# Kernel optimization log

Hardware: AMD Instinct MI355X
Metric: run time of the kernel (lower is better)

Reference implementation:

```python
import jax, jax.numpy as jnp
import numpy as np

N = 100000          # number of nodes (queries == sources here)
DEG = 32            # uniform neighbor count
E = N * DEG         # total edges
C_IN = 8
HID = 32
C_OUT = 32


def setup_inputs() -> dict:
    key = jax.random.key(0)
    k1, k2, k3, k4, k5 = jax.random.split(key, 5)
    in_features = jax.random.normal(k1, (N, C_IN), dtype=jnp.float32)
    in_weights = jax.random.uniform(k2, (N,), dtype=jnp.float32)
    # MLP: Linear(2*C_IN -> HID), GELU, Linear(HID -> C_OUT)
    W1 = jax.random.normal(k3, (2 * C_IN, HID), dtype=jnp.float32) / np.sqrt(2 * C_IN)
    b1 = jnp.zeros((HID,), dtype=jnp.float32)
    W2 = jax.random.normal(k4, (HID, C_OUT), dtype=jnp.float32) / np.sqrt(HID)
    b2 = jnp.zeros((C_OUT,), dtype=jnp.float32)
    neighbor_index = jax.random.randint(k5, (E,), 0, N, dtype=jnp.int64)
    row_splits = (jnp.arange(N + 1, dtype=jnp.int64) * DEG)  # uniform CSR splits
    return {"in_features": in_features, "in_weights": in_weights,
            "W1": W1, "b1": b1, "W2": W2, "b2": b2,
            "neighbor_index": neighbor_index, "row_splits": row_splits}


def reference(in_features, in_weights, W1, b1, W2, b2, neighbor_index, row_splits):
    num_edges = neighbor_index.shape[0]
    num_out = row_splits.shape[0] - 1  # M output nodes
    # segment id of each edge (== repeat_interleave of node ids by row counts)
    seg = jnp.searchsorted(row_splits, jnp.arange(num_edges), side="right") - 1
    gathered = in_features[neighbor_index]          # [E, C_in] neighbor gather
    self_feats = in_features[seg]                   # [E, C_in] repeated self features
    agg = jnp.concatenate([gathered, self_feats], axis=1)  # [E, 2*C_in]
    h = jax.nn.gelu(agg @ W1 + b1)                  # [E, HID]
    h = h @ W2 + b2                                 # [E, C_out]
    h = in_weights[neighbor_index][:, None] * h     # quadrature weighting
    sums = jax.ops.segment_sum(h, seg, num_segments=num_out)  # segment_csr sum
    counts = (row_splits[1:] - row_splits[:-1]).astype(h.dtype)
    out = sums / jnp.maximum(counts, 1)[:, None]    # reduce='mean'
    return out
```

## Files before the change

kernel.cpp:

```cpp
#include <hip/hip_runtime.h>

#define DEG 32
#define HID 32
#define CIN 8

typedef float v2f __attribute__((ext_vector_type(2)));
typedef short bf16x8 __attribute__((ext_vector_type(8)));
typedef float f32x16 __attribute__((ext_vector_type(16)));

#define GELU_A ((float)(2.0 * 1.4426950408889634 * 0.7978845608028654))
#define GELU_B ((float)(2.0 * 1.4426950408889634 * 0.7978845608028654 * 0.044715))

__device__ __forceinline__ unsigned f2bf(float f) {
    unsigned b = __float_as_uint(f);
    return (b + 0x7fffu + ((b >> 16) & 1u)) >> 16;
}
__device__ __forceinline__ unsigned pack2(float lo, float hi) {
    return f2bf(lo) | (f2bf(hi) << 16);
}

__global__ __launch_bounds__(256) void precompute_xw(
    const float* __restrict__ x, const float* __restrict__ W1,
    const float* __restrict__ W2, unsigned* __restrict__ x16,
    unsigned* __restrict__ w1f, unsigned* __restrict__ w2f, int N) {
    int tid = blockIdx.x * 256 + threadIdx.x;
    if (blockIdx.x == 0) {
        int t = threadIdx.x;
        if (t < 64) {
            int kb = (t >> 5) * 8, col = t & 31;
            uint4 o;
            o.x = pack2(W1[(kb + 0) * HID + col], W1[(kb + 1) * HID + col]);
            o.y = pack2(W1[(kb + 2) * HID + col], W1[(kb + 3) * HID + col]);
            o.z = pack2(W1[(kb + 4) * HID + col], W1[(kb + 5) * HID + col]);
            o.w = pack2(W1[(kb + 6) * HID + col], W1[(kb + 7) * HID + col]);
            *(uint4*)(w1f + t * 4) = o;
        } else if (t < 192) {
            int u = t - 64;
            int f = u >> 6, l = u & 63;
            int kb = f * 16 + ((l >> 5) * 8), col = l & 31;
            uint4 o;
            o.x = pack2(W2[(kb + 0) * HID + col], W2[(kb + 1) * HID + col]);
            o.y = pack2(W2[(kb + 2) * HID + col], W2[(kb + 3) * HID + col]);
            o.z = pack2(W2[(kb + 4) * HID + col], W2[(kb + 5) * HID + col]);
            o.w = pack2(W2[(kb + 6) * HID + col], W2[(kb + 7) * HID + col]);
            *(uint4*)(w2f + (f * 64 + l) * 4) = o;
        }
    }
    if (tid < N) {
        const float4* xp = (const float4*)(x + (size_t)tid * CIN);
        float4 a = xp[0], b = xp[1];
        uint4 o;
        o.x = pack2(a.x, a.y);  o.y = pack2(a.z, a.w);
        o.z = pack2(b.x, b.y);  o.w = pack2(b.z, b.w);
        *(uint4*)(x16 + (size_t)tid * 4) = o;
    }
}

__device__ __forceinline__ float gelu_reduce(const f32x16& acc, const float* swp,
                                             float b1v) {
    float4 wq0 = *(const float4*)(swp);
    float4 wq1 = *(const float4*)(swp + 8);
    float4 wq2 = *(const float4*)(swp + 16);
    float4 wq3 = *(const float4*)(swp + 24);
    float wqa[16] = {wq0.x, wq0.y, wq0.z, wq0.w,  wq1.x, wq1.y, wq1.z, wq1.w,
                     wq2.x, wq2.y, wq2.z, wq2.w,  wq3.x, wq3.y, wq3.z, wq3.w};
    v2f gacc = {0.f, 0.f};
#pragma unroll
    for (int i = 0; i < 16; i += 2) {
        v2f tt = {acc[i] + b1v, acc[i + 1] + b1v};
        v2f x2 = tt * tt;
        v2f zz = tt * (x2 * (-GELU_B) + (-GELU_A));
        v2f ee;
        ee.x = __builtin_amdgcn_exp2f(zz.x);  ee.y = __builtin_amdgcn_exp2f(zz.y);
        v2f dd = ee + 1.0f;
        v2f rr;
        rr.x = __builtin_amdgcn_rcpf(dd.x);   rr.y = __builtin_amdgcn_rcpf(dd.y);
        v2f wp = {wqa[i], wqa[i + 1]};
        gacc += wp * (tt * rr);
    }
    float g = gacc.x + gacc.y;
    g += __shfl_xor(g, 32);
    return g;
}

__global__ __launch_bounds__(256, 5) void git_fused(
    const unsigned* __restrict__ x16, const unsigned* __restrict__ w1f,
    const unsigned* __restrict__ w2f, const float* __restrict__ wgt,
    const float* __restrict__ b1, const float* __restrict__ b2,
    const int* __restrict__ nbr, float* __restrict__ out, int N) {
    __shared__ float          sw[8 * DEG];
    __shared__ unsigned short sg[32 * 40];
    __shared__ float          sws[32];

    int t = threadIdx.x;
    int wv = t >> 6;
    int l  = t & 63;
    int l5 = l & 31;
    int hi = l >> 5;
    int nb = blockIdx.x * 8 + wv * 2;

    int jn[2]; float w[2]; int ncl[2];
#pragma unroll
    for (int r = 0; r < 2; ++r) {
        int n = nb + r; ncl[r] = n < N ? n : (N - 1);
        jn[r] = nbr[ncl[r] * DEG + l5];
        w[r]  = wgt[jn[r]];
    }
    if (hi == 0) {
#pragma unroll
        for (int r = 0; r < 2; ++r) sw[(wv * 2 + r) * DEG + l5] = w[r];
    }

    float ws[2];
#pragma unroll
    for (int r = 0; r < 2; ++r) {
        float s = w[r];
        s += __shfl_xor(s, 1);  s += __shfl_xor(s, 2);
        s += __shfl_xor(s, 4);  s += __shfl_xor(s, 8);
        s += __shfl_xor(s, 16);
        ws[r] = s;
    }

    bf16x8 af0 = *((const bf16x8*)x16 + (hi ? ncl[0] : jn[0]));
    bf16x8 af1 = *((const bf16x8*)x16 + (hi ? ncl[1] : jn[1]));
    bf16x8 bf  = *((const bf16x8*)w1f + l);
    float myb1 = b1[l5];

    f32x16 z0 = {}, z1 = {};
    f32x16 a0 = __builtin_amdgcn_mfma_f32_32x32x16_bf16(af0, bf, z0, 0, 0, 0);
    f32x16 a1 = __builtin_amdgcn_mfma_f32_32x32x16_bf16(af1, bf, z1, 0, 0, 0);

    const float* swb = &sw[wv * 2 * DEG + hi * 4];
    float g0 = gelu_reduce(a0, swb, myb1);
    float g1 = gelu_reduce(a1, swb + DEG, myb1);

    if (hi == 0) {
        sg[(wv * 2 + 0) * 40 + l5] = (unsigned short)f2bf(g0);
        sg[(wv * 2 + 1) * 40 + l5] = (unsigned short)f2bf(g1);
        if (l5 == 0) { sws[wv * 2] = ws[0]; sws[wv * 2 + 1] = ws[1]; }
    }

    __syncthreads();

    if (wv != 0) return;

    const char* sgb = (const char*)sg;
    bf16x8 ea1 = *(const bf16x8*)(sgb + l5 * 80 + hi * 16);
    bf16x8 ea2 = *(const bf16x8*)(sgb + l5 * 80 + 32 + hi * 16);
    bf16x8 eb1 = *((const bf16x8*)w2f + l);
    bf16x8 eb2 = *((const bf16x8*)w2f + 64 + l);

    f32x16 zz = {};
    f32x16 acc = __builtin_amdgcn_mfma_f32_32x32x16_bf16(ea1, eb1, zz, 0, 0, 0);
    acc = __builtin_amdgcn_mfma_f32_32x32x16_bf16(ea2, eb2, acc, 0, 0, 0);

    float myb2 = b2[l5];
    float4 wsq = *(const float4*)(sws + hi * 4);
    float wsa[4] = {wsq.x, wsq.y, wsq.z, wsq.w};

#pragma unroll
    for (int i = 0; i < 4; ++i) {
        int r = i + 4 * hi;
        int node = blockIdx.x * 8 + r;
        if (node < N)
            out[(size_t)node * HID + l5] = fmaf(wsa[i], myb2, acc[i]) * (1.0f / DEG);
    }
}

__global__ __launch_bounds__(256) void fused_fallback(
    const float* __restrict__ x, const float* __restrict__ wgt,
    const float* __restrict__ W1, const float* __restrict__ b1,
    const float* __restrict__ W2, const float* __restrict__ b2,
    const int* __restrict__ nbr, float* __restrict__ out, int N) {
    __shared__ float sW2[HID * HID];
    __shared__ float sb2[HID];
    __shared__ int2  sp[8 * DEG];
    int t = threadIdx.x;
#pragma unroll
    for (int i = 0; i < 4; ++i) sW2[t + i * 256] = W2[t + i * 256];
    if (t < HID) sb2[t] = b2[t];
    int slot = t >> 5, hid = t & 31;
    int node = blockIdx.x * 8 + slot;
    bool valid = node < N;
    int nc = valid ? node : (N - 1);
    int   j_own = nbr[nc * DEG + hid];
    float w_own = wgt[j_own];
    sp[slot * DEG + hid] = make_int2(j_own * (CIN * 4), __float_as_int(w_own));
    const float4* xip = (const float4*)(x + (size_t)nc * CIN);
    float4 xa = xip[0], xb = xip[1];
    float w1t[8];
#pragma unroll
    for (int k = 0; k < 8; ++k) w1t[k] = W1[k * HID + hid];
    float vb = b1[hid];
    vb = fmaf(xa.x, W1[ 8 * HID + hid], vb);
    vb = fmaf(xa.y, W1[ 9 * HID + hid], vb);
    vb = fmaf(xa.z, W1[10 * HID + hid], vb);
    vb = fmaf(xa.w, W1[11 * HID + hid], vb);
    vb = fmaf(xb.x, W1[12 * HID + hid], vb);
    vb = fmaf(xb.y, W1[13 * HID + hid], vb);
    vb = fmaf(xb.z, W1[14 * HID + hid], vb);
    vb = fmaf(xb.w, W1[15 * HID + hid], vb);
    float ws = w_own;
    ws += __shfl_xor(ws, 1);  ws += __shfl_xor(ws, 2);
    ws += __shfl_xor(ws, 4);  ws += __shfl_xor(ws, 8);
    ws += __shfl_xor(ws, 16);
    __syncthreads();
    const char* xbytes = (const char*)x;
    const int2* myp = &sp[slot * DEG];
    float g = 0.f;
#pragma unroll 8
    for (int e = 0; e < DEG; ++e) {
        int2  p  = myp[e];
        float wjv = __int_as_float(p.y);
        const float4* xjp = (const float4*)(xbytes + (unsigned)p.x);
        float4 a = xjp[0], b = xjp[1];
        float tin = vb;
        tin = fmaf(a.x, w1t[0], tin); tin = fmaf(a.y, w1t[1], tin);
        tin = fmaf(a.z, w1t[2], tin); tin = fmaf(a.w, w1t[3], tin);
        tin = fmaf(b.x, w1t[4], tin); tin = fmaf(b.y, w1t[5], tin);
        tin = fmaf(b.z, w1t[6], tin); tin = fmaf(b.w, w1t[7], tin);
        float x2 = tin * tin;
        float z  = tin * fmaf(GELU_B, x2, GELU_A);
        float e2 = __builtin_amdgcn_exp2f(z);
        float r  = __builtin_amdgcn_rcpf(1.0f + e2);
        g = fmaf(wjv, fmaf(-tin, r, tin), g);
    }
    float acc = 0.f;
#pragma unroll
    for (int h = 0; h < HID; ++h) {
        float gh = __shfl(g, h, 32);
        acc = fmaf(gh, sW2[h * HID + hid], acc);
    }
    if (valid) out[(size_t)node * HID + hid] = fmaf(ws, sb2[hid], acc) * (1.0f / DEG);
}

extern "C" void kernel_launch(void* const* d_in, const int* in_sizes, int n_in,
                              void* d_out, int out_size, void* d_ws, size_t ws_size,
                              hipStream_t stream) {
    const float* x   = (const float*)d_in[0];
    const float* wq  = (const float*)d_in[1];
    const float* W1  = (const float*)d_in[2];
    const float* b1  = (const float*)d_in[3];
    const float* W2  = (const float*)d_in[4];
    const float* b2  = (const float*)d_in[5];
    const int*   nbr = (const int*)d_in[6];
    float* out = (float*)d_out;

    int N = in_sizes[1];

    size_t off_x16 = 0;
    size_t off_w1  = (off_x16 + (size_t)N * 16 + 255) & ~(size_t)255;
    size_t off_w2  = off_w1 + 1024;
    size_t need    = off_w2 + 2048;

    if (ws_size >= need) {
        unsigned* x16 = (unsigned*)((char*)d_ws + off_x16);
        unsigned* w1f = (unsigned*)((char*)d_ws + off_w1);
        unsigned* w2f = (unsigned*)((char*)d_ws + off_w2);

        int blocks_pre = (N + 255) / 256;
        precompute_xw<<<blocks_pre, 256, 0, stream>>>(x, W1, W2, x16, w1f, w2f, N);

        int blocks_main = (N + 7) / 8;
        git_fused<<<blocks_main, 256, 0, stream>>>(x16, w1f, w2f, wq, b1, b2,
                                                   nbr, out, N);
    } else {
        int blocks = (N + 7) / 8;
        fused_fallback<<<blocks, 256, 0, stream>>>(x, wq, W1, b1, W2, b2, nbr, out, N);
    }
}
```

Measured before the change: 113.0 us.

## Make git_fused a persistent grid-stride kernel with prefetch and double-buffered LDS

The fused kernel now runs on a capped grid of 2048 blocks. Each block loops over 8-node groups in grid-stride order. While it computes the current group, it issues the neighbor-index, weight and feature gathers for the next group and the index load for the one after. The shared-memory buffers for the second MLP stage are double-buffered, and the wave that does the second-stage MFMA rotates per group, so one barrier per iteration is enough. The aim is to hide gather latency and avoid per-block launch and setup cost, in exchange for more live registers and dropping the min-waves occupancy hint.

Result: slower. 119.6 us (+5.8%).

```diff
diff --git a/kernel.cpp b/kernel.cpp
--- a/kernel.cpp
+++ b/kernel.cpp
@@ -58,112 +58,137 @@
 
 __device__ __forceinline__ float gelu_reduce(const f32x16& acc, const float* swp,
                                              float b1v) {
-    float4 wq0 = *(const float4*)(swp);
-    float4 wq1 = *(const float4*)(swp + 8);
-    float4 wq2 = *(const float4*)(swp + 16);
-    float4 wq3 = *(const float4*)(swp + 24);
-    float wqa[16] = {wq0.x, wq0.y, wq0.z, wq0.w,  wq1.x, wq1.y, wq1.z, wq1.w,
-                     wq2.x, wq2.y, wq2.z, wq2.w,  wq3.x, wq3.y, wq3.z, wq3.w};
     v2f gacc = {0.f, 0.f};
 #pragma unroll
-    for (int i = 0; i < 16; i += 2) {
-        v2f tt = {acc[i] + b1v, acc[i + 1] + b1v};
-        v2f x2 = tt * tt;
-        v2f zz = tt * (x2 * (-GELU_B) + (-GELU_A));
-        v2f ee;
-        ee.x = __builtin_amdgcn_exp2f(zz.x);  ee.y = __builtin_amdgcn_exp2f(zz.y);
-        v2f dd = ee + 1.0f;
-        v2f rr;
-        rr.x = __builtin_amdgcn_rcpf(dd.x);   rr.y = __builtin_amdgcn_rcpf(dd.y);
-        v2f wp = {wqa[i], wqa[i + 1]};
-        gacc += wp * (tt * rr);
+    for (int q = 0; q < 4; ++q) {
+        float4 wq = *(const float4*)(swp + 8 * q);
+#pragma unroll
+        for (int h = 0; h < 2; ++h) {
+            int i = q * 4 + h * 2;
+            v2f tt = {acc[i] + b1v, acc[i + 1] + b1v};
+            v2f x2 = tt * tt;
+            v2f zz = tt * (x2 * (-GELU_B) + (-GELU_A));
+            v2f ee;
+            ee.x = __builtin_amdgcn_exp2f(zz.x);  ee.y = __builtin_amdgcn_exp2f(zz.y);
+            v2f dd = ee + 1.0f;
+            v2f rr;
+            rr.x = __builtin_amdgcn_rcpf(dd.x);   rr.y = __builtin_amdgcn_rcpf(dd.y);
+            v2f wp = h ? (v2f){wq.z, wq.w} : (v2f){wq.x, wq.y};
+            gacc += wp * (tt * rr);
+        }
     }
     float g = gacc.x + gacc.y;
     g += __shfl_xor(g, 32);
     return g;
 }
 
-__global__ __launch_bounds__(256, 5) void git_fused(
+__global__ __launch_bounds__(256) void git_fused(
     const unsigned* __restrict__ x16, const unsigned* __restrict__ w1f,
     const unsigned* __restrict__ w2f, const float* __restrict__ wgt,
     const float* __restrict__ b1, const float* __restrict__ b2,
     const int* __restrict__ nbr, float* __restrict__ out, int N) {
-    __shared__ float          sw[8 * DEG];
-    __shared__ unsigned short sg[32 * 40];
-    __shared__ float          sws[32];
-
+    __shared__ float sw[8 * DEG];
+    __shared__ __align__(16) unsigned short sg[2][32 * 40];
+    __shared__ __align__(16) float          sws[2][8];
+
+    const int ngroups = (N + 7) >> 3;
     int t = threadIdx.x;
     int wv = t >> 6;
     int l  = t & 63;
     int l5 = l & 31;
     int hi = l >> 5;
-    int nb = blockIdx.x * 8 + wv * 2;
-
-    int jn[2]; float w[2]; int ncl[2];
-#pragma unroll
-    for (int r = 0; r < 2; ++r) {
-        int n = nb + r; ncl[r] = n < N ? n : (N - 1);
-        jn[r] = nbr[ncl[r] * DEG + l5];
-        w[r]  = wgt[jn[r]];
-    }
-    if (hi == 0) {
-#pragma unroll
-        for (int r = 0; r < 2; ++r) sw[(wv * 2 + r) * DEG + l5] = w[r];
-    }
-
-    float ws[2];
-#pragma unroll
-    for (int r = 0; r < 2; ++r) {
-        float s = w[r];
-        s += __shfl_xor(s, 1);  s += __shfl_xor(s, 2);
-        s += __shfl_xor(s, 4);  s += __shfl_xor(s, 8);
-        s += __shfl_xor(s, 16);
-        ws[r] = s;
-    }
-
-    bf16x8 af0 = *((const bf16x8*)x16 + (hi ? ncl[0] : jn[0]));
-    bf16x8 af1 = *((const bf16x8*)x16 + (hi ? ncl[1] : jn[1]));
-    bf16x8 bf  = *((const bf16x8*)w1f + l);
-    float myb1 = b1[l5];
-
-    f32x16 z0 = {}, z1 = {};
-    f32x16 a0 = __builtin_amdgcn_mfma_f32_32x32x16_bf16(af0, bf, z0, 0, 0, 0);
-    f32x16 a1 = __builtin_amdgcn_mfma_f32_32x32x16_bf16(af1, bf, z1, 0, 0, 0);
-
-    const float* swb = &sw[wv * 2 * DEG + hi * 4];
-    float g0 = gelu_reduce(a0, swb, myb1);
-    float g1 = gelu_reduce(a1, swb + DEG, myb1);
-
-    if (hi == 0) {
-        sg[(wv * 2 + 0) * 40 + l5] = (unsigned short)f2bf(g0);
-        sg[(wv * 2 + 1) * 40 + l5] = (unsigned short)f2bf(g1);
-        if (l5 == 0) { sws[wv * 2] = ws[0]; sws[wv * 2 + 1] = ws[1]; }
-    }
-
-    __syncthreads();
-
-    if (wv != 0) return;
-
-    const char* sgb = (const char*)sg;
-    bf16x8 ea1 = *(const bf16x8*)(sgb + l5 * 80 + hi * 16);
-    bf16x8 ea2 = *(const bf16x8*)(sgb + l5 * 80 + 32 + hi * 16);
-    bf16x8 eb1 = *((const bf16x8*)w2f + l);
-    bf16x8 eb2 = *((const bf16x8*)w2f + 64 + l);
-
-    f32x16 zz = {};
-    f32x16 acc = __builtin_amdgcn_mfma_f32_32x32x16_bf16(ea1, eb1, zz, 0, 0, 0);
-    acc = __builtin_amdgcn_mfma_f32_32x32x16_bf16(ea2, eb2, acc, 0, 0, 0);
-
-    float myb2 = b2[l5];
-    float4 wsq = *(const float4*)(sws + hi * 4);
-    float wsa[4] = {wsq.x, wsq.y, wsq.z, wsq.w};
-
-#pragma unroll
-    for (int i = 0; i < 4; ++i) {
-        int r = i + 4 * hi;
-        int node = blockIdx.x * 8 + r;
-        if (node < N)
-            out[(size_t)node * HID + l5] = fmaf(wsa[i], myb2, acc[i]) * (1.0f / DEG);
+
+    bf16x8 bfrag = *((const bf16x8*)w1f + l);
+    bf16x8 eb1   = *((const bf16x8*)w2f + l);
+    bf16x8 eb2   = *((const bf16x8*)w2f + 64 + l);
+    float  myb1  = b1[l5];
+    float  myb2  = b2[l5];
+    const bf16x8* x16v = (const bf16x8*)x16;
+
+    int g = blockIdx.x;
+    const int gstep = gridDim.x;
+    if (g >= ngroups) return;
+
+    int nb0 = g * 8 + wv * 2;
+    int n0c = min(nb0, N - 1), n1c = min(nb0 + 1, N - 1);
+    int   J = nbr[(hi ? n1c : n0c) * DEG + l5];
+    float W = wgt[J];
+    int jsw = __shfl_xor(J, 32);
+    bf16x8 A0 = x16v[hi ? n0c : J];
+    bf16x8 A1 = x16v[hi ? n1c : jsw];
+
+    int gn = g + gstep;
+    int Jn = 0;
+    if (gn < ngroups) {
+        int nbn = gn * 8 + wv * 2;
+        Jn = nbr[min(nbn + hi, N - 1) * DEG + l5];
+    }
+
+    int p = 0;
+    while (true) {
+        bf16x8 A0n, A1n;
+        float  Wn = 0.f;
+        int gn2 = gn + gstep;
+        int Jn2 = 0;
+        if (gn < ngroups) {
+            int nbn = gn * 8 + wv * 2;
+            int n0n = min(nbn, N - 1), n1n = min(nbn + 1, N - 1);
+            Wn = wgt[Jn];
+            int jswn = __shfl_xor(Jn, 32);
+            A0n = x16v[hi ? n0n : Jn];
+            A1n = x16v[hi ? n1n : jswn];
+            if (gn2 < ngroups) {
+                Jn2 = nbr[min(gn2 * 8 + wv * 2 + hi, N - 1) * DEG + l5];
+            }
+        }
+
+        float ws = W;
+        ws += __shfl_xor(ws, 1);  ws += __shfl_xor(ws, 2);
+        ws += __shfl_xor(ws, 4);  ws += __shfl_xor(ws, 8);
+        ws += __shfl_xor(ws, 16);
+        sw[(wv * 2 + hi) * DEG + l5] = W;
+        if (l5 == 0) sws[p][wv * 2 + hi] = ws;
+
+        f32x16 z0 = {}, z1 = {};
+        f32x16 a0 = __builtin_amdgcn_mfma_f32_32x32x16_bf16(A0, bfrag, z0, 0, 0, 0);
+        f32x16 a1 = __builtin_amdgcn_mfma_f32_32x32x16_bf16(A1, bfrag, z1, 0, 0, 0);
+
+        const float* swb = &sw[wv * 2 * DEG + hi * 4];
+        float g0 = gelu_reduce(a0, swb, myb1);
+        float g1 = gelu_reduce(a1, swb + DEG, myb1);
+
+        if (hi == 0) {
+            sg[p][(wv * 2 + 0) * 40 + l5] = (unsigned short)f2bf(g0);
+            sg[p][(wv * 2 + 1) * 40 + l5] = (unsigned short)f2bf(g1);
+        }
+
+        __syncthreads();
+
+        if (wv == (g & 3)) {
+            const char* sgb = (const char*)sg[p];
+            bf16x8 ea1 = *(const bf16x8*)(sgb + l5 * 80 + hi * 16);
+            bf16x8 ea2 = *(const bf16x8*)(sgb + l5 * 80 + 32 + hi * 16);
+            f32x16 zz = {};
+            f32x16 acc = __builtin_amdgcn_mfma_f32_32x32x16_bf16(ea1, eb1, zz, 0, 0, 0);
+            acc = __builtin_amdgcn_mfma_f32_32x32x16_bf16(ea2, eb2, acc, 0, 0, 0);
+
+            float4 wsq = *(const float4*)(&sws[p][hi * 4]);
+            float wsa[4] = {wsq.x, wsq.y, wsq.z, wsq.w};
+#pragma unroll
+            for (int i = 0; i < 4; ++i) {
+                int r = i + 4 * hi;
+                int node = g * 8 + r;
+                if (node < N)
+                    out[(size_t)node * HID + l5] =
+                        fmaf(wsa[i], myb2, acc[i]) * (1.0f / DEG);
+            }
+        }
+
+        if (gn >= ngroups) break;
+        g = gn;  gn = gn2;
+        J = Jn;  Jn = Jn2;
+        W = Wn;  A0 = A0n;  A1 = A1n;
+        p ^= 1;
     }
 }
 
@@ -261,7 +286,8 @@
         int blocks_pre = (N + 255) / 256;
         precompute_xw<<<blocks_pre, 256, 0, stream>>>(x, W1, W2, x16, w1f, w2f, N);
 
-        int blocks_main = (N + 7) / 8;
+        int ngroups = (N + 7) / 8;
+        int blocks_main = ngroups < 2048 ? ngroups : 2048;
         git_fused<<<blocks_main, 256, 0, stream>>>(x16, w1f, w2f, wq, b1, b2,
                                                    nbr, out, N);
     } else {
```

## Give each wave four nodes and do the second MLP layer per wave without block sync

Applied to the files above, without the earlier changes.

Each wavefront now handles four output nodes instead of two, using both 32-lane halves to load neighbor indices for different nodes, so the block covers 16 nodes. The second-layer MFMA is done per wave from wave-private shared memory, which removes the __syncthreads and the idle waves that previously exited while wave 0 finished alone. W2 fragments and biases are hoisted to the start, and launch bounds drop to 4 blocks per SM. In exchange each wave does more MFMA and output work and holds more registers, and occupancy may fall.

Measured after the change: 115.8 us. 1.02x slower.

```diff
diff --git a/kernel.cpp b/kernel.cpp
--- a/kernel.cpp
+++ b/kernel.cpp
@@ -58,112 +58,116 @@
 
 __device__ __forceinline__ float gelu_reduce(const f32x16& acc, const float* swp,
                                              float b1v) {
-    float4 wq0 = *(const float4*)(swp);
-    float4 wq1 = *(const float4*)(swp + 8);
-    float4 wq2 = *(const float4*)(swp + 16);
-    float4 wq3 = *(const float4*)(swp + 24);
-    float wqa[16] = {wq0.x, wq0.y, wq0.z, wq0.w,  wq1.x, wq1.y, wq1.z, wq1.w,
-                     wq2.x, wq2.y, wq2.z, wq2.w,  wq3.x, wq3.y, wq3.z, wq3.w};
     v2f gacc = {0.f, 0.f};
 #pragma unroll
-    for (int i = 0; i < 16; i += 2) {
-        v2f tt = {acc[i] + b1v, acc[i + 1] + b1v};
-        v2f x2 = tt * tt;
-        v2f zz = tt * (x2 * (-GELU_B) + (-GELU_A));
-        v2f ee;
-        ee.x = __builtin_amdgcn_exp2f(zz.x);  ee.y = __builtin_amdgcn_exp2f(zz.y);
-        v2f dd = ee + 1.0f;
-        v2f rr;
-        rr.x = __builtin_amdgcn_rcpf(dd.x);   rr.y = __builtin_amdgcn_rcpf(dd.y);
-        v2f wp = {wqa[i], wqa[i + 1]};
-        gacc += wp * (tt * rr);
+    for (int q = 0; q < 4; ++q) {
+        float4 wq = *(const float4*)(swp + 8 * q);
+#pragma unroll
+        for (int h = 0; h < 2; ++h) {
+            int i = q * 4 + h * 2;
+            v2f tt = {acc[i] + b1v, acc[i + 1] + b1v};
+            v2f x2 = tt * tt;
+            v2f zz = tt * (x2 * (-GELU_B) + (-GELU_A));
+            v2f ee;
+            ee.x = __builtin_amdgcn_exp2f(zz.x);  ee.y = __builtin_amdgcn_exp2f(zz.y);
+            v2f dd = ee + 1.0f;
+            v2f rr;
+            rr.x = __builtin_amdgcn_rcpf(dd.x);   rr.y = __builtin_amdgcn_rcpf(dd.y);
+            v2f wp = h ? (v2f){wq.z, wq.w} : (v2f){wq.x, wq.y};
+            gacc += wp * (tt * rr);
+        }
     }
     float g = gacc.x + gacc.y;
     g += __shfl_xor(g, 32);
     return g;
 }
 
-__global__ __launch_bounds__(256, 5) void git_fused(
+__global__ __launch_bounds__(256, 4) void git_fused(
     const unsigned* __restrict__ x16, const unsigned* __restrict__ w1f,
     const unsigned* __restrict__ w2f, const float* __restrict__ wgt,
     const float* __restrict__ b1, const float* __restrict__ b2,
     const int* __restrict__ nbr, float* __restrict__ out, int N) {
-    __shared__ float          sw[8 * DEG];
-    __shared__ unsigned short sg[32 * 40];
-    __shared__ float          sws[32];
+    __shared__ float sw[4 * 4 * 32];
+    __shared__ __align__(16) unsigned short sg[1792];
 
     int t = threadIdx.x;
     int wv = t >> 6;
     int l  = t & 63;
     int l5 = l & 31;
     int hi = l >> 5;
-    int nb = blockIdx.x * 8 + wv * 2;
-
-    int jn[2]; float w[2]; int ncl[2];
-#pragma unroll
-    for (int r = 0; r < 2; ++r) {
-        int n = nb + r; ncl[r] = n < N ? n : (N - 1);
-        jn[r] = nbr[ncl[r] * DEG + l5];
-        w[r]  = wgt[jn[r]];
-    }
-    if (hi == 0) {
-#pragma unroll
-        for (int r = 0; r < 2; ++r) sw[(wv * 2 + r) * DEG + l5] = w[r];
-    }
-
-    float ws[2];
-#pragma unroll
-    for (int r = 0; r < 2; ++r) {
-        float s = w[r];
-        s += __shfl_xor(s, 1);  s += __shfl_xor(s, 2);
-        s += __shfl_xor(s, 4);  s += __shfl_xor(s, 8);
-        s += __shfl_xor(s, 16);
-        ws[r] = s;
-    }
-
-    bf16x8 af0 = *((const bf16x8*)x16 + (hi ? ncl[0] : jn[0]));
-    bf16x8 af1 = *((const bf16x8*)x16 + (hi ? ncl[1] : jn[1]));
-    bf16x8 bf  = *((const bf16x8*)w1f + l);
+    int nb = blockIdx.x * 16 + wv * 4;
+
+    int n0 = min(nb + 0, N - 1), n1 = min(nb + 1, N - 1);
+    int n2 = min(nb + 2, N - 1), n3 = min(nb + 3, N - 1);
+
+    int JA = nbr[(hi ? n1 : n0) * DEG + l5];
+    int JB = nbr[(hi ? n3 : n2) * DEG + l5];
+    float WA = wgt[JA];
+    float WB = wgt[JB];
+    int jswA = __shfl_xor(JA, 32);
+    int jswB = __shfl_xor(JB, 32);
+
+    const bf16x8* x16v = (const bf16x8*)x16;
+    bf16x8 A0 = x16v[hi ? n0 : JA];
+    bf16x8 A1 = x16v[hi ? n1 : jswA];
+    bf16x8 A2 = x16v[hi ? n2 : JB];
+    bf16x8 A3 = x16v[hi ? n3 : jswB];
+    bf16x8 bfrag = *((const bf16x8*)w1f + l);
+    bf16x8 eb1   = *((const bf16x8*)w2f + l);
+    bf16x8 eb2   = *((const bf16x8*)w2f + 64 + l);
     float myb1 = b1[l5];
+    float myb2 = b2[l5];
+
+    float* swv = &sw[wv * 128];
+    swv[hi * 32 + l5]      = WA;
+    swv[64 + hi * 32 + l5] = WB;
+
+    float wsA = WA, wsB = WB;
+    wsA += __shfl_xor(wsA, 1);  wsA += __shfl_xor(wsA, 2);
+    wsA += __shfl_xor(wsA, 4);  wsA += __shfl_xor(wsA, 8);
+    wsA += __shfl_xor(wsA, 16);
+    wsB += __shfl_xor(wsB, 1);  wsB += __shfl_xor(wsB, 2);
+    wsB += __shfl_xor(wsB, 4);  wsB += __shfl_xor(wsB, 8);
+    wsB += __shfl_xor(wsB, 16);
 
     f32x16 z0 = {}, z1 = {};
-    f32x16 a0 = __builtin_amdgcn_mfma_f32_32x32x16_bf16(af0, bf, z0, 0, 0, 0);
-    f32x16 a1 = __builtin_amdgcn_mfma_f32_32x32x16_bf16(af1, bf, z1, 0, 0, 0);
-
-    const float* swb = &sw[wv * 2 * DEG + hi * 4];
-    float g0 = gelu_reduce(a0, swb, myb1);
-    float g1 = gelu_reduce(a1, swb + DEG, myb1);
-
-    if (hi == 0) {
-        sg[(wv * 2 + 0) * 40 + l5] = (unsigned short)f2bf(g0);
-        sg[(wv * 2 + 1) * 40 + l5] = (unsigned short)f2bf(g1);
-        if (l5 == 0) { sws[wv * 2] = ws[0]; sws[wv * 2 + 1] = ws[1]; }
-    }
-
-    __syncthreads();
-
-    if (wv != 0) return;
-
-    const char* sgb = (const char*)sg;
+    f32x16 a0 = __builtin_amdgcn_mfma_f32_32x32x16_bf16(A0, bfrag, z0, 0, 0, 0);
+    f32x16 a1 = __builtin_amdgcn_mfma_f32_32x32x16_bf16(A1, bfrag, z1, 0, 0, 0);
+    float g0 = gelu_reduce(a0, swv + hi * 4,      myb1);
+    float g1 = gelu_reduce(a1, swv + 32 + hi * 4, myb1);
+    f32x16 z2 = {}, z3 = {};
+    f32x16 a2 = __builtin_amdgcn_mfma_f32_32x32x16_bf16(A2, bfrag, z2, 0, 0, 0);
+    f32x16 a3 = __builtin_amdgcn_mfma_f32_32x32x16_bf16(A3, bfrag, z3, 0, 0, 0);
+    float g2 = gelu_reduce(a2, swv + 64 + hi * 4, myb1);
+    float g3 = gelu_reduce(a3, swv + 96 + hi * 4, myb1);
+
+    unsigned short* sgw = &sg[wv * 160];
+    float ga = hi ? g2 : g0;
+    float gb = hi ? g3 : g1;
+    sgw[(2 * hi + 0) * 40 + l5] = (unsigned short)f2bf(ga);
+    sgw[(2 * hi + 1) * 40 + l5] = (unsigned short)f2bf(gb);
+
+    float wsa[4];
+    wsa[0] = __shfl(wsA, 0);
+    wsa[1] = __shfl(wsA, 32);
+    wsa[2] = __shfl(wsB, 0);
+    wsa[3] = __shfl(wsB, 32);
+
+    const char* sgb = (const char*)sgw;
     bf16x8 ea1 = *(const bf16x8*)(sgb + l5 * 80 + hi * 16);
     bf16x8 ea2 = *(const bf16x8*)(sgb + l5 * 80 + 32 + hi * 16);
-    bf16x8 eb1 = *((const bf16x8*)w2f + l);
-    bf16x8 eb2 = *((const bf16x8*)w2f + 64 + l);
-
     f32x16 zz = {};
     f32x16 acc = __builtin_amdgcn_mfma_f32_32x32x16_bf16(ea1, eb1, zz, 0, 0, 0);
     acc = __builtin_amdgcn_mfma_f32_32x32x16_bf16(ea2, eb2, acc, 0, 0, 0);
 
-    float myb2 = b2[l5];
-    float4 wsq = *(const float4*)(sws + hi * 4);
-    float wsa[4] = {wsq.x, wsq.y, wsq.z, wsq.w};
-
-#pragma unroll
-    for (int i = 0; i < 4; ++i) {
-        int r = i + 4 * hi;
-        int node = blockIdx.x * 8 + r;
-        if (node < N)
-            out[(size_t)node * HID + l5] = fmaf(wsa[i], myb2, acc[i]) * (1.0f / DEG);
+    if (hi == 0) {
+#pragma unroll
+        for (int i = 0; i < 4; ++i) {
+            int node = nb + i;
+            if (node < N)
+                out[(size_t)node * HID + l5] =
+                    fmaf(wsa[i], myb2, acc[i]) * (1.0f / DEG);
+        }
     }
 }
 
@@ -261,7 +265,7 @@
         int blocks_pre = (N + 255) / 256;
         precompute_xw<<<blocks_pre, 256, 0, stream>>>(x, W1, W2, x16, w1f, w2f, N);
 
-        int blocks_main = (N + 7) / 8;
+        int blocks_main = (N + 15) / 16;
         git_fused<<<blocks_main, 256, 0, stream>>>(x16, w1f, w2f, wq, b1, b2,
                                                    nbr, out, N);
     } else {
```
